# Optimization experiments

Hardware: AMD Instinct MI355X
Metric: run time of the kernel (lower is better)

Reference implementation:

```python
import jax, jax.numpy as jnp
import numpy as np

D_MODEL = 1024
NUM_HEADS = 16
D_HEAD = D_MODEL // NUM_HEADS
NEG_BIG = 10000000000.0  # matches the torch module's -1e10 mask constant


def setup_inputs() -> dict:
    key = jax.random.key(0)
    ks = jax.random.split(key, 9)
    d = D_MODEL
    scale = 1.0 / np.sqrt(d)
    inp = {
        "x": jax.random.normal(ks[0], (2, 2048, d), dtype=jnp.float32),
        "W_q": jax.random.normal(ks[1], (d, d), dtype=jnp.float32) * scale,
        "b_q": jnp.zeros((d,), dtype=jnp.float32),
        "W_k": jax.random.normal(ks[2], (d, d), dtype=jnp.float32) * scale,
        "b_k": jnp.zeros((d,), dtype=jnp.float32),
        "W_v": jax.random.normal(ks[3], (d, d), dtype=jnp.float32) * scale,
        "b_v": jnp.zeros((d,), dtype=jnp.float32),
        "W_o": jax.random.normal(ks[4], (d, d), dtype=jnp.float32) * scale,
        "b_o": jnp.zeros((d,), dtype=jnp.float32),
    }
    return inp


def reference(x, W_q, b_q, W_k, b_k, W_v, b_v, W_o, b_o):
    B, S, d = x.shape
    H, Dh = NUM_HEADS, D_HEAD

    Q = x @ W_q + b_q  # [B,S,d]
    K = x @ W_k + b_k
    V = x @ W_v + b_v

    # split heads: [B,S,d] -> [B,H,S,Dh]
    Qh = Q.reshape(B, S, H, Dh).transpose(0, 2, 1, 3)
    Kh = K.reshape(B, S, H, Dh).transpose(0, 2, 1, 3)
    Vh = V.reshape(B, S, H, Dh).transpose(0, 2, 1, 3)

    scores = jnp.einsum("bhid,bhjd->bhij", Qh, Kh) / jnp.sqrt(
        jnp.asarray(Dh, dtype=x.dtype)
    )

    # causal mask: tril(scores) - 1e10 * (1 - tril_mask)
    causal = jnp.tril(jnp.ones((S, S), dtype=x.dtype))
    scores = scores * causal - NEG_BIG * (1.0 - causal)

    attn = jax.nn.softmax(scores, axis=-1)  # dropout p=0.0 -> identity

    vals = jnp.einsum("bhij,bhjd->bhid", attn, Vh)  # [B,H,S,Dh]
    vals = vals.transpose(0, 2, 1, 3).reshape(B, S, d)

    return vals @ W_o + b_o
```

## Files before the change

### kernel.cpp

```cpp
#include <hip/hip_runtime.h>

typedef unsigned short u16;
typedef __attribute__((ext_vector_type(8))) short short8;
typedef __attribute__((ext_vector_type(4))) short shortx4;
typedef __attribute__((ext_vector_type(4))) float floatx4;

#define S_ 2048
#define D_ 1024
#define DQKV_ 3072
#define H_ 16
#define DH_ 64

#define EXP2F(x) __builtin_amdgcn_exp2f(x)

template <bool B> struct BoolC { static constexpr bool value = B; };

__device__ __forceinline__ float bf2f(u16 x) {
    union { unsigned int u; float f; } v; v.u = ((unsigned int)x) << 16; return v.f;
}
__device__ __forceinline__ u16 f2bf(float f) {
    unsigned int u = __float_as_uint(f);
    return (u16)((u + 0x7fffu + ((u >> 16) & 1u)) >> 16);
}
__device__ __forceinline__ unsigned int cvtpk_bf16(float lo, float hi) {
    unsigned int r;
    asm("v_cvt_pk_bf16_f32 %0, %1, %2" : "=v"(r) : "v"(lo), "v"(hi));
    return r;
}

__device__ __forceinline__ void async16(const void* g, void* l) {
    __builtin_amdgcn_global_load_lds(
        (const __attribute__((address_space(1))) unsigned int*)g,
        (__attribute__((address_space(3))) unsigned int*)l, 16, 0, 0);
}

__global__ __launch_bounds__(256) void convert_x(const float* __restrict__ x, u16* __restrict__ xb) {
    const size_t i = ((size_t)blockIdx.x * 256 + threadIdx.x) * 4;
    float4 v = *(const float4*)&x[i];
    shortx4 h;
    h[0] = (short)f2bf(v.x); h[1] = (short)f2bf(v.y);
    h[2] = (short)f2bf(v.z); h[3] = (short)f2bf(v.w);
    *(shortx4*)&xb[i] = h;
}

__global__ __launch_bounds__(256) void transpose_w4(const float* __restrict__ Wq, const float* __restrict__ Wk,
                                                    const float* __restrict__ Wv, const float* __restrict__ Wo,
                                                    u16* __restrict__ Wqkvt, u16* __restrict__ Wot) {
    __shared__ u16 tile[32][33];
    const int z = blockIdx.z;
    const float* W = (z == 0) ? Wq : (z == 1) ? Wk : (z == 2) ? Wv : Wo;
    u16* dst = (z == 3) ? Wot : (Wqkvt + (size_t)z * D_ * D_);
    const int tx = threadIdx.x, ty = threadIdx.y;
    const int n0 = blockIdx.x * 32, k0 = blockIdx.y * 32;
#pragma unroll
    for (int r = 0; r < 4; ++r) {
        int k = ty + r * 8;
        tile[k][tx] = f2bf(W[(size_t)(k0 + k) * D_ + n0 + tx]);
    }
    __syncthreads();
#pragma unroll
    for (int r = 0; r < 4; ++r) {
        int n = ty + r * 8;
        dst[(size_t)(n0 + n) * D_ + k0 + tx] = tile[tx][n];
    }
}

__global__ __launch_bounds__(256) void transpose_headV(const u16* __restrict__ QKV, u16* __restrict__ Vt) {
    __shared__ u16 tile[64 * 65];
    const int t = threadIdx.x;
    const int bh = blockIdx.y, b = bh >> 4, h = bh & 15;
    const int s0 = blockIdx.x << 6;
#pragma unroll
    for (int i = 0; i < 16; ++i) {
        int idx = t + (i << 8);
        int s = idx >> 6, d = idx & 63;
        tile[s * 65 + d] = QKV[(size_t)(b * S_ + s0 + s) * DQKV_ + 2048 + h * DH_ + d];
    }
    __syncthreads();
#pragma unroll
    for (int i = 0; i < 16; ++i) {
        int idx = t + (i << 8);
        int d = idx >> 6, p = idx & 63;
        int sk = ((p >> 5) << 5) | (((p >> 2) & 1) << 4) | (((p >> 3) & 3) << 2) | (p & 3);
        Vt[((size_t)bh * DH_ + d) * S_ + s0 + p] = tile[sk * 65 + d];
    }
}

template <int BM, int BN, bool OUTF32>
__global__ __launch_bounds__(256) void gemm_bt(const u16* __restrict__ A, const u16* __restrict__ Bt,
                                               const float* __restrict__ b0, const float* __restrict__ b1,
                                               const float* __restrict__ b2, void* __restrict__ Cp,
                                               int M, int N, int Kd) {
    constexpr int FI = BM / 32, FJ = BN / 32;
    __shared__ __align__(16) u16 smem[2][(BM + BN) * 32];
    const int t = threadIdx.x;

    const int nwg = gridDim.x * gridDim.y;
    int fid = blockIdx.y * gridDim.x + blockIdx.x;
    if ((nwg & 7) == 0) fid = (fid & 7) * (nwg >> 3) + (fid >> 3);
    const int bx = fid % gridDim.x, by = fid / gridDim.x;
    const int m0 = by * BM, n0 = bx * BN;

    const int w = t >> 6, lane = t & 63;
    const int lr = lane & 15, lg = lane >> 4;
    const int wm = (w >> 1) * (BM / 2), wn = (w & 1) * (BN / 2);
    const int srow = lane >> 2, scol = (lane & 3) << 3;
    floatx4 acc[FI][FJ] = {};

    auto stage = [&](int buf, int k0) {
        u16* As = &smem[buf][0];
        u16* Bs = &smem[buf][BM * 32];
#pragma unroll
        for (int c = 0; c < BM / 64; ++c) {
            int rbase = (w * (BM / 64) + c) * 16;
            async16(&A[(size_t)(m0 + rbase + srow) * Kd + k0 + scol], &As[rbase * 32]);
        }
#pragma unroll
        for (int c = 0; c < BN / 64; ++c) {
            int rbase = (w * (BN / 64) + c) * 16;
            async16(&Bt[(size_t)(n0 + rbase + srow) * Kd + k0 + scol], &Bs[rbase * 32]);
        }
    };

    stage(0, 0);
    const int nk = Kd / 32;
    for (int kk = 0; kk < nk; ++kk) {
        const int cur = kk & 1;
        __syncthreads();
        if (kk + 1 < nk) stage(cur ^ 1, (kk + 1) * 32);
        const u16* As = &smem[cur][0];
        const u16* Bs = &smem[cur][BM * 32];

        short8 af[FI], bfr[FJ];
#pragma unroll
        for (int i = 0; i < FI; ++i) af[i]  = *(const short8*)&As[(wm + i * 16 + lr) * 32 + lg * 8];
#pragma unroll
        for (int j = 0; j < FJ; ++j) bfr[j] = *(const short8*)&Bs[(wn + j * 16 + lr) * 32 + lg * 8];
#pragma unroll
        for (int i = 0; i < FI; ++i)
#pragma unroll
            for (int j = 0; j < FJ; ++j)
                acc[i][j] = __builtin_amdgcn_mfma_f32_16x16x32_bf16(af[i], bfr[j], acc[i][j], 0, 0, 0);
    }

    if (!OUTF32) {
        __syncthreads();
        u16* Cs = &smem[0][0];
#pragma unroll
        for (int j = 0; j < FJ; ++j) {
            int c = wn + j * 16 + lr;
            int col = n0 + c;
            const float* bp = (col < 1024) ? b0 : (col < 2048) ? b1 : b2;
            float bv = bp[col & 1023];
#pragma unroll
            for (int i = 0; i < FI; ++i)
#pragma unroll
                for (int ii = 0; ii < 4; ++ii) {
                    int r = wm + i * 16 + lg * 4 + ii;
                    Cs[r * BN + (c ^ ((r & 15) << 3))] = f2bf(acc[i][j][ii] + bv);
                }
        }
        __syncthreads();
        constexpr int CPR = BN / 8;
        constexpr int ITER = BM * CPR / 256;
#pragma unroll
        for (int it = 0; it < ITER; ++it) {
            int g = it * 256 + t;
            int r = g / CPR, cc = g % CPR;
            short8 vv = *(const short8*)&Cs[r * BN + ((cc * 8) ^ ((r & 15) << 3))];
            *(short8*)((u16*)Cp + (size_t)(m0 + r) * N + n0 + cc * 8) = vv;
        }
    } else {
#pragma unroll
        for (int j = 0; j < FJ; ++j) {
            int col = n0 + wn + j * 16 + lr;
            const float* bp = (col < 1024) ? b0 : (col < 2048) ? b1 : b2;
            float bv = bp[col & 1023];
#pragma unroll
            for (int i = 0; i < FI; ++i) {
                int rb = m0 + wm + i * 16 + lg * 4;
#pragma unroll
                for (int ii = 0; ii < 4; ++ii)
                    ((float*)Cp)[(size_t)(rb + ii) * N + col] = acc[i][j][ii] + bv;
            }
        }
    }
}

__global__ __launch_bounds__(256) void attn_mfma(const u16* __restrict__ QKV, const u16* __restrict__ Vt,
                                                 u16* __restrict__ O) {
    __shared__ __align__(16) u16 KsA[2][64 * 64];
    __shared__ __align__(16) u16 VsA[2][64 * 64];
    const int t = threadIdx.x, w = t >> 6, lane = t & 63;
    const int lr = lane & 15, lg = lane >> 4;
    const int bh = blockIdx.x, b = bh >> 4, h = bh & 15;
    const int qt = 31 - blockIdx.y;
    const int q0 = qt << 6;
    const float cs = 0.18033688f;

    const u16* Kb  = QKV + (size_t)b * S_ * DQKV_ + 1024 + h * DH_;
    const u16* Vtb = Vt + (size_t)bh * DH_ * S_;

    const int rb = lane >> 3;
    const int cc = ((lane & 7) ^ rb) << 3;
    const int swz = lr & 7;

    short8 qf[2];
#pragma unroll
    for (int ks = 0; ks < 2; ++ks)
        qf[ks] = *(const short8*)&QKV[(size_t)(b * S_ + q0 + w * 16 + lr) * DQKV_ + h * DH_ + ks * 32 + lg * 8];

    floatx4 of[4] = {};
    float lsum = 0.f;

    auto stage = [&](int buf, int kbase) {
        u16* Kd = &KsA[buf][w * 512];
        u16* Vd = &VsA[buf][w * 512];
        async16(&Kb[(size_t)(kbase + w * 8 + rb) * DQKV_ + cc], Kd);
        async16(&Kb[(size_t)(kbase + 32 + w * 8 + rb) * DQKV_ + cc], Kd + 2048);
        async16(&Vtb[(size_t)(w * 8 + rb) * S_ + kbase + cc], Vd);
        async16(&Vtb[(size_t)(32 + w * 8 + rb) * S_ + kbase + cc], Vd + 2048);
    };

    stage(0, 0);

    auto body = [&](int kb, auto diagc) {
        constexpr bool DIAG = decltype(diagc)::value;
        const int cur = kb & 1;
        __syncthreads();
        if (kb < qt) stage(cur ^ 1, (kb + 1) << 6);
        const u16* Kc = KsA[cur];
        const u16* Vc = VsA[cur];

        floatx4 sf[4] = {};
        __builtin_amdgcn_s_setprio(1);
#pragma unroll
        for (int ks = 0; ks < 2; ++ks)
#pragma unroll
            for (int tt = 0; tt < 4; ++tt) {
                short8 kf = *(const short8*)&Kc[(tt * 16 + lr) * 64 + ((((ks << 2) + lg) ^ swz) << 3)];
                sf[tt] = __builtin_amdgcn_mfma_f32_16x16x32_bf16(kf, qf[ks], sf[tt], 0, 0, 0);
            }
        __builtin_amdgcn_s_setprio(0);

        float ev[4][4];
#pragma unroll
        for (int tt = 0; tt < 4; ++tt) {
            float s0;
#pragma unroll
            for (int ii = 0; ii < 4; ++ii) {
                float e = EXP2F(sf[tt][ii] * cs);
                if (DIAG && (tt * 16 + lg * 4 + ii > w * 16 + lr)) e = 0.f;
                ev[tt][ii] = e;
                s0 = (ii == 0) ? e : s0 + e;
            }
            lsum += s0;
        }

        __builtin_amdgcn_s_setprio(1);
#pragma unroll
        for (int ks = 0; ks < 2; ++ks) {
            union { short8 s; unsigned int u[4]; } pk;
            pk.u[0] = cvtpk_bf16(ev[2 * ks][0], ev[2 * ks][1]);
            pk.u[1] = cvtpk_bf16(ev[2 * ks][2], ev[2 * ks][3]);
            pk.u[2] = cvtpk_bf16(ev[2 * ks + 1][0], ev[2 * ks + 1][1]);
            pk.u[3] = cvtpk_bf16(ev[2 * ks + 1][2], ev[2 * ks + 1][3]);
#pragma unroll
            for (int tt = 0; tt < 4; ++tt) {
                short8 vf = *(const short8*)&Vc[(tt * 16 + lr) * 64 + ((((ks << 2) + lg) ^ swz) << 3)];
                of[tt] = __builtin_amdgcn_mfma_f32_16x16x32_bf16(pk.s, vf, of[tt], 0, 0, 0);
            }
        }
        __builtin_amdgcn_s_setprio(0);
    };

    for (int kb = 0; kb < qt; ++kb) body(kb, BoolC<false>{});
    body(qt, BoolC<true>{});

    lsum += __shfl_xor(lsum, 16);
    lsum += __shfl_xor(lsum, 32);
    const float rinv = 1.f / lsum;
    float rv[4];
#pragma unroll
    for (int ii = 0; ii < 4; ++ii)
        rv[ii] = __shfl(rinv, (lane & 48) | (lg * 4 + ii));

#pragma unroll
    for (int tt = 0; tt < 4; ++tt)
#pragma unroll
        for (int ii = 0; ii < 4; ++ii)
            O[(size_t)(b * S_ + q0 + w * 16 + lg * 4 + ii) * D_ + h * DH_ + tt * 16 + lr] =
                f2bf(of[tt][ii] * rv[ii]);
}

extern "C" void kernel_launch(void* const* d_in, const int* in_sizes, int n_in,
                              void* d_out, int out_size, void* d_ws, size_t ws_size,
                              hipStream_t stream) {
    (void)in_sizes; (void)n_in; (void)out_size; (void)ws_size;
    const float* x  = (const float*)d_in[0];
    const float* Wq = (const float*)d_in[1];
    const float* bq = (const float*)d_in[2];
    const float* Wk = (const float*)d_in[3];
    const float* bk = (const float*)d_in[4];
    const float* Wv = (const float*)d_in[5];
    const float* bv = (const float*)d_in[6];
    const float* Wo = (const float*)d_in[7];
    const float* bo = (const float*)d_in[8];

    u16* ws    = (u16*)d_ws;
    u16* WqkvT = ws;
    u16* WoT   = ws + (size_t)3 * (1 << 20);
    u16* QKV   = ws + (size_t)4 * (1 << 20);
    u16* Vtm   = ws + (size_t)16 * (1 << 20);
    u16* xbf   = ws + (size_t)20 * (1 << 20);
    u16* Am    = ws + (size_t)20 * (1 << 20);

    convert_x<<<4096, 256, 0, stream>>>(x, xbf);
    transpose_w4<<<dim3(32, 32, 4), dim3(32, 8), 0, stream>>>(Wq, Wk, Wv, Wo, WqkvT, WoT);

    gemm_bt<128, 128, false><<<dim3(DQKV_ / 128, 4096 / 128), 256, 0, stream>>>(
        xbf, WqkvT, bq, bk, bv, QKV, 4096, DQKV_, 1024);

    transpose_headV<<<dim3(32, 32), 256, 0, stream>>>(QKV, Vtm);

    attn_mfma<<<dim3(32, 32), 256, 0, stream>>>(QKV, Vtm, Am);

    gemm_bt<64, 128, true><<<dim3(1024 / 128, 4096 / 64), 256, 0, stream>>>(
        Am, WoT, bo, bo, bo, d_out, 4096, 1024, 1024);
}
```

Before: 179.4 us.

## Split attention key block across wave pairs, reuse K/V fragments, reorder q-tiles

Each wave now handles 32 query rows against half of the 64-key block instead of 16 rows against all keys. Every K and V fragment read from shared memory therefore feeds two MFMAs, which halves LDS read traffic per MFMA. The partial outputs and row sums from the two key halves are combined through shared memory at the end. The block-to-q-tile mapping is also permuted to balance causal work across CUs, and launch bounds now request 4 blocks per CU. The cost is an extra shared-memory reduction step and more register pressure.

```diff
diff --git a/kernel.cpp b/kernel.cpp
--- a/kernel.cpp
+++ b/kernel.cpp
@@ -187,39 +187,46 @@
     }
 }
 
-__global__ __launch_bounds__(256) void attn_mfma(const u16* __restrict__ QKV, const u16* __restrict__ Vt,
-                                                 u16* __restrict__ O) {
+__global__ __launch_bounds__(256, 4) void attn_mfma(const u16* __restrict__ QKV, const u16* __restrict__ Vt,
+                                                    u16* __restrict__ O) {
     __shared__ __align__(16) u16 KsA[2][64 * 64];
     __shared__ __align__(16) u16 VsA[2][64 * 64];
     const int t = threadIdx.x, w = t >> 6, lane = t & 63;
     const int lr = lane & 15, lg = lane >> 4;
+    const int wq = w & 1, wk = w >> 1;
     const int bh = blockIdx.x, b = bh >> 4, h = bh & 15;
-    const int qt = 31 - blockIdx.y;
+    const int ya = blockIdx.y & 7, yb = blockIdx.y >> 3;
+    const int a4 = (ya + 4) & 7;
+    const int cq = (yb == 0) ? ya : (yb == 1) ? (7 - ya) : (yb == 2) ? a4 : (7 - a4);
+    const int qt = (yb << 3) + cq;
     const int q0 = qt << 6;
     const float cs = 0.18033688f;
 
     const u16* Kb  = QKV + (size_t)b * S_ * DQKV_ + 1024 + h * DH_;
     const u16* Vtb = Vt + (size_t)bh * DH_ * S_;
 
-    const int rb = lane >> 3;
-    const int cc = ((lane & 7) ^ rb) << 3;
+    const int rb8 = lane >> 3;
+    const int cc = ((lane & 7) ^ rb8) << 3;
     const int swz = lr & 7;
 
-    short8 qf[2];
-#pragma unroll
-    for (int ks = 0; ks < 2; ++ks)
-        qf[ks] = *(const short8*)&QKV[(size_t)(b * S_ + q0 + w * 16 + lr) * DQKV_ + h * DH_ + ks * 32 + lg * 8];
-
-    floatx4 of[4] = {};
-    float lsum = 0.f;
+    short8 qf[2][2];
+#pragma unroll
+    for (int qs = 0; qs < 2; ++qs)
+#pragma unroll
+        for (int ks = 0; ks < 2; ++ks)
+            qf[qs][ks] = *(const short8*)&QKV[(size_t)(b * S_ + q0 + wq * 32 + qs * 16 + lr) * DQKV_ +
+                                              h * DH_ + ks * 32 + lg * 8];
+
+    floatx4 of[2][4] = {};
+    float lsum[2] = {0.f, 0.f};
 
     auto stage = [&](int buf, int kbase) {
         u16* Kd = &KsA[buf][w * 512];
         u16* Vd = &VsA[buf][w * 512];
-        async16(&Kb[(size_t)(kbase + w * 8 + rb) * DQKV_ + cc], Kd);
-        async16(&Kb[(size_t)(kbase + 32 + w * 8 + rb) * DQKV_ + cc], Kd + 2048);
-        async16(&Vtb[(size_t)(w * 8 + rb) * S_ + kbase + cc], Vd);
-        async16(&Vtb[(size_t)(32 + w * 8 + rb) * S_ + kbase + cc], Vd + 2048);
+        async16(&Kb[(size_t)(kbase + w * 8 + rb8) * DQKV_ + cc], Kd);
+        async16(&Kb[(size_t)(kbase + 32 + w * 8 + rb8) * DQKV_ + cc], Kd + 2048);
+        async16(&Vtb[(size_t)(w * 8 + rb8) * S_ + kbase + cc], Vd);
+        async16(&Vtb[(size_t)(32 + w * 8 + rb8) * S_ + kbase + cc], Vd + 2048);
     };
 
     stage(0, 0);
@@ -232,44 +239,49 @@
         const u16* Kc = KsA[cur];
         const u16* Vc = VsA[cur];
 
-        floatx4 sf[4] = {};
+        floatx4 sf[2][2] = {};
         __builtin_amdgcn_s_setprio(1);
 #pragma unroll
         for (int ks = 0; ks < 2; ++ks)
 #pragma unroll
-            for (int tt = 0; tt < 4; ++tt) {
-                short8 kf = *(const short8*)&Kc[(tt * 16 + lr) * 64 + ((((ks << 2) + lg) ^ swz) << 3)];
-                sf[tt] = __builtin_amdgcn_mfma_f32_16x16x32_bf16(kf, qf[ks], sf[tt], 0, 0, 0);
+            for (int tt = 0; tt < 2; ++tt) {
+                short8 kf = *(const short8*)&Kc[(wk * 32 + tt * 16 + lr) * 64 + ((((ks << 2) + lg) ^ swz) << 3)];
+                sf[0][tt] = __builtin_amdgcn_mfma_f32_16x16x32_bf16(kf, qf[0][ks], sf[0][tt], 0, 0, 0);
+                sf[1][tt] = __builtin_amdgcn_mfma_f32_16x16x32_bf16(kf, qf[1][ks], sf[1][tt], 0, 0, 0);
             }
         __builtin_amdgcn_s_setprio(0);
 
-        float ev[4][4];
-#pragma unroll
-        for (int tt = 0; tt < 4; ++tt) {
-            float s0;
-#pragma unroll
-            for (int ii = 0; ii < 4; ++ii) {
-                float e = EXP2F(sf[tt][ii] * cs);
-                if (DIAG && (tt * 16 + lg * 4 + ii > w * 16 + lr)) e = 0.f;
-                ev[tt][ii] = e;
-                s0 = (ii == 0) ? e : s0 + e;
+        float ev[2][2][4];
+#pragma unroll
+        for (int qs = 0; qs < 2; ++qs)
+#pragma unroll
+            for (int tt = 0; tt < 2; ++tt) {
+                float s0;
+#pragma unroll
+                for (int ii = 0; ii < 4; ++ii) {
+                    float e = EXP2F(sf[qs][tt][ii] * cs);
+                    if (DIAG && (wk * 32 + tt * 16 + lg * 4 + ii > wq * 32 + qs * 16 + lr)) e = 0.f;
+                    ev[qs][tt][ii] = e;
+                    s0 = (ii == 0) ? e : s0 + e;
+                }
+                lsum[qs] += s0;
             }
-            lsum += s0;
-        }
-
+
+        short8 vfr[4];
+#pragma unroll
+        for (int ttd = 0; ttd < 4; ++ttd)
+            vfr[ttd] = *(const short8*)&Vc[(ttd * 16 + lr) * 64 + ((((wk << 2) + lg) ^ swz) << 3)];
         __builtin_amdgcn_s_setprio(1);
 #pragma unroll
-        for (int ks = 0; ks < 2; ++ks) {
+        for (int qs = 0; qs < 2; ++qs) {
             union { short8 s; unsigned int u[4]; } pk;
-            pk.u[0] = cvtpk_bf16(ev[2 * ks][0], ev[2 * ks][1]);
-            pk.u[1] = cvtpk_bf16(ev[2 * ks][2], ev[2 * ks][3]);
-            pk.u[2] = cvtpk_bf16(ev[2 * ks + 1][0], ev[2 * ks + 1][1]);
-            pk.u[3] = cvtpk_bf16(ev[2 * ks + 1][2], ev[2 * ks + 1][3]);
-#pragma unroll
-            for (int tt = 0; tt < 4; ++tt) {
-                short8 vf = *(const short8*)&Vc[(tt * 16 + lr) * 64 + ((((ks << 2) + lg) ^ swz) << 3)];
-                of[tt] = __builtin_amdgcn_mfma_f32_16x16x32_bf16(pk.s, vf, of[tt], 0, 0, 0);
-            }
+            pk.u[0] = cvtpk_bf16(ev[qs][0][0], ev[qs][0][1]);
+            pk.u[1] = cvtpk_bf16(ev[qs][0][2], ev[qs][0][3]);
+            pk.u[2] = cvtpk_bf16(ev[qs][1][0], ev[qs][1][1]);
+            pk.u[3] = cvtpk_bf16(ev[qs][1][2], ev[qs][1][3]);
+#pragma unroll
+            for (int ttd = 0; ttd < 4; ++ttd)
+                of[qs][ttd] = __builtin_amdgcn_mfma_f32_16x16x32_bf16(pk.s, vfr[ttd], of[qs][ttd], 0, 0, 0);
         }
         __builtin_amdgcn_s_setprio(0);
     };
@@ -277,20 +289,50 @@
     for (int kb = 0; kb < qt; ++kb) body(kb, BoolC<false>{});
     body(qt, BoolC<true>{});
 
-    lsum += __shfl_xor(lsum, 16);
-    lsum += __shfl_xor(lsum, 32);
-    const float rinv = 1.f / lsum;
-    float rv[4];
-#pragma unroll
-    for (int ii = 0; ii < 4; ++ii)
-        rv[ii] = __shfl(rinv, (lane & 48) | (lg * 4 + ii));
-
-#pragma unroll
-    for (int tt = 0; tt < 4; ++tt)
-#pragma unroll
-        for (int ii = 0; ii < 4; ++ii)
-            O[(size_t)(b * S_ + q0 + w * 16 + lg * 4 + ii) * D_ + h * DH_ + tt * 16 + lr] =
-                f2bf(of[tt][ii] * rv[ii]);
+    __syncthreads();
+    float* mb = (float*)&KsA[0][0];
+    float* lb = (float*)&VsA[0][0];
+    if (wk == 1) {
+        float* mw = mb + wq * 2048;
+#pragma unroll
+        for (int qs = 0; qs < 2; ++qs)
+#pragma unroll
+            for (int ttd = 0; ttd < 4; ++ttd)
+                *(floatx4*)&mw[(qs * 4 + ttd) * 256 + lane * 4] = of[qs][ttd];
+        lb[wq * 128 + lane * 2 + 0] = lsum[0];
+        lb[wq * 128 + lane * 2 + 1] = lsum[1];
+    }
+    __syncthreads();
+    if (wk == 0) {
+        float* mw = mb + wq * 2048;
+#pragma unroll
+        for (int qs = 0; qs < 2; ++qs)
+#pragma unroll
+            for (int ttd = 0; ttd < 4; ++ttd)
+                of[qs][ttd] += *(const floatx4*)&mw[(qs * 4 + ttd) * 256 + lane * 4];
+        lsum[0] += lb[wq * 128 + lane * 2 + 0];
+        lsum[1] += lb[wq * 128 + lane * 2 + 1];
+
+        float rv[2][4];
+#pragma unroll
+        for (int qs = 0; qs < 2; ++qs) {
+            float s = lsum[qs];
+            s += __shfl_xor(s, 16);
+            s += __shfl_xor(s, 32);
+            float rinv = 1.f / s;
+#pragma unroll
+            for (int ii = 0; ii < 4; ++ii)
+                rv[qs][ii] = __shfl(rinv, (lane & 48) | (lg * 4 + ii));
+        }
+#pragma unroll
+        for (int qs = 0; qs < 2; ++qs)
+#pragma unroll
+            for (int ttd = 0; ttd < 4; ++ttd)
+#pragma unroll
+                for (int ii = 0; ii < 4; ++ii)
+                    O[(size_t)(b * S_ + q0 + wq * 32 + qs * 16 + lg * 4 + ii) * D_ + h * DH_ + ttd * 16 + lr] =
+                        f2bf(of[qs][ttd][ii] * rv[qs][ii]);
+    }
 }
 
 extern "C" void kernel_launch(void* const* d_in, const int* in_sizes, int n_in,
```

Result: no change. 178.5 us (-0.5%).
